# Performance work log

Measured on AMD Instinct MI355X. Metric: run time of the kernel, lower is better.

The kernel has to match this reference:

```python
import jax, jax.numpy as jnp
import numpy as np

B, S, V = 2, 336, 8      # batch, seq_len, n_vars
D, H, P = 256, 8, 96     # d_model, num_heads, pred_len
DK = D // H
OUT_CHN = 8
EPS = 1e-5


def _layernorm(x, g, b):
    mu = jnp.mean(x, axis=-1, keepdims=True)
    var = jnp.var(x, axis=-1, keepdims=True)
    return (x - mu) * jax.lax.rsqrt(var + EPS) * g + b


def _attn_ff(src, Wq, bq, Wk, bk, Wv, bv, Wo, bo, ln1_g, ln1_b):
    # src: [N, L, D]; manual MHA + residual + layernorm (dropout=0)
    N, L, _ = src.shape
    q = (src @ Wq + bq).reshape(N, L, H, DK).transpose(0, 2, 1, 3)
    k = (src @ Wk + bk).reshape(N, L, H, DK).transpose(0, 2, 1, 3)
    v = (src @ Wv + bv).reshape(N, L, H, DK).transpose(0, 2, 1, 3)
    scores = jnp.einsum('nhqd,nhkd->nhqk', q, k) / np.sqrt(DK).astype(np.float32)
    attn = jax.nn.softmax(scores, axis=-1)
    o = jnp.einsum('nhqk,nhkd->nhqd', attn, v)
    o = o.transpose(0, 2, 1, 3).reshape(N, L, D) @ Wo + bo
    return _layernorm(src + o, ln1_g, ln1_b)


def setup_inputs() -> dict:
    key = jax.random.key(0)
    ks = jax.random.split(key, 8)
    s = 1.0 / np.sqrt(D)
    return {
        'x': jax.random.normal(ks[0], (B, S, V), dtype=jnp.float32),
        'emb_w': jax.random.normal(ks[1], (1, D), dtype=jnp.float32),
        'emb_b': jnp.zeros((D,), jnp.float32),
        'Wq': jax.random.normal(ks[2], (D, D), dtype=jnp.float32) * s,
        'bq': jnp.zeros((D,), jnp.float32),
        'Wk': jax.random.normal(ks[3], (D, D), dtype=jnp.float32) * s,
        'bk': jnp.zeros((D,), jnp.float32),
        'Wv': jax.random.normal(ks[4], (D, D), dtype=jnp.float32) * s,
        'bv': jnp.zeros((D,), jnp.float32),
        'Wo': jax.random.normal(ks[5], (D, D), dtype=jnp.float32) * s,
        'bo': jnp.zeros((D,), jnp.float32),
        'ln1_g': jnp.ones((D,), jnp.float32),
        'ln1_b': jnp.zeros((D,), jnp.float32),
        'norm_g': jnp.ones((D,), jnp.float32),
        'norm_b': jnp.zeros((D,), jnp.float32),
        'proj_w': jax.random.normal(ks[6], (S * D, P), dtype=jnp.float32) / np.sqrt(S * D).astype(np.float32),
        'proj_b': jnp.zeros((P,), jnp.float32),
    }


def reference(x, emb_w, emb_b, Wq, bq, Wk, bk, Wv, bv, Wo, bo,
              ln1_g, ln1_b, norm_g, norm_b, proj_w, proj_b):
    attn_p = (Wq, bq, Wk, bk, Wv, bv, Wo, bo, ln1_g, ln1_b)
    # x: [B,S,V] -> [B,V,S] -> embed each scalar to D
    e = x.transpose(0, 2, 1)[..., None] @ emb_w + emb_b  # [B,V,S,D]
    for _ in range(10):
        # attention over time axis (shared weights)
        e = _attn_ff(e.reshape(B * V, S, D), *attn_p).reshape(B, V, S, D)
        e = _layernorm(e.transpose(0, 2, 1, 3), norm_g, norm_b)  # [B,S,V,D]
        # attention over variable axis (same weights)
        e = _attn_ff(e.reshape(B * S, V, D), *attn_p).reshape(B, S, V, D)
        e = e.transpose(0, 2, 1, 3)  # [B,V,S,D]
    out = e.reshape(B, V, S * D) @ proj_w + proj_b  # [B,V,P]
    return out.transpose(0, 2, 1)[:, :, :OUT_CHN]  # [B,P,out_chn]
```

## Files before the change

### kernel.cpp

```cpp
#include <hip/hip_runtime.h>

#define SS 336
#define VV 8
#define DD 256
#define DKK 32
#define NTOK 5376
#define NTD (NTOK * DD)
#define ATT_SCALE 0.17677669529663687f
#define LN_EPS 1e-5f

typedef _Float16 f16x8 __attribute__((ext_vector_type(8)));
typedef _Float16 f16x4v __attribute__((ext_vector_type(4)));
typedef __attribute__((ext_vector_type(4))) float f32x4;

__device__ inline _Float16 f2h(float f) { return (_Float16)f; }

__global__ __launch_bounds__(256) void k_prep_w(
    const float* __restrict__ Wq, const float* __restrict__ Wk,
    const float* __restrict__ Wv, const float* __restrict__ Wo,
    _Float16* __restrict__ WT2) {
  int z = blockIdx.y;
  const float* W = (z == 0) ? Wq : (z == 1) ? Wk : (z == 2) ? Wv : Wo;
  int o = blockIdx.x * 256 + threadIdx.x;
  int blk = o >> 9;
  int idx = o & 511;
  int lane = idx >> 3, j = idx & 7;
  int nt = blk >> 3, kb = blk & 7;
  int lcol = lane & 15, quad = lane >> 4;
  int n = nt * 16 + lcol;
  int k = kb * 32 + quad * 8 + j;
  WT2[(size_t)z * 65536 + o] = f2h(W[k * 256 + n]);
}

__global__ __launch_bounds__(256) void k_embed(
    const float* __restrict__ x, const float* __restrict__ ew,
    const float* __restrict__ eb, float* __restrict__ E,
    _Float16* __restrict__ E16) {
  int token = blockIdx.x;
  int n = token / SS, s = token - n * SS;
  int b = n >> 3, v = n & 7;
  float xv = x[(b * SS + s) * VV + v];
  int d = threadIdx.x;
  float val = fmaf(xv, ew[d], eb[d]);
  E[token * DD + d] = val;
  E16[token * DD + d] = f2h(val);
}

#define KSTR 36
#define VTSTR 344
#define PSTR 72
#define QSTR 40
__global__ __launch_bounds__(512) void k_attn_time(
    const _Float16* __restrict__ Et16, const _Float16* __restrict__ WT2,
    const float* __restrict__ bq, const float* __restrict__ bk,
    const float* __restrict__ bv, _Float16* __restrict__ O16) {
  int qg = blockIdx.x, h = blockIdx.y, n = blockIdx.z;
  int tid = threadIdx.x;
  int wave = tid >> 6, lane = tid & 63;
  int quad = lane >> 4, lcol = lane & 15;

  __shared__ __align__(16) char SMRAW[143264];
  _Float16* Ks  = (_Float16*)SMRAW;
  _Float16* Vt  = (_Float16*)(SMRAW + 24192);
  _Float16* Qs  = (_Float16*)(SMRAW + 46240);
  _Float16* Wl  = (_Float16*)(SMRAW + 60320);
  _Float16* Ach = (_Float16*)(SMRAW + 109472);
  _Float16* PsB = (_Float16*)(SMRAW + 60320);

  const size_t ebase = (size_t)(n * SS) * DD;
  const size_t base  = ebase + h * DKK;
  int qt0 = qg ? 11 : 0;
  int qtend = qg ? 21 : 11;

  const f32x4 z4 = {0.f, 0.f, 0.f, 0.f};

  {
    int h2 = h * 2;
    for (int c = tid; c < 3072; c += 512) {
      int ot = c >> 9, rest = c & 511;
      int z = (ot < 2) ? 1 : (ot < 4) ? 2 : 0;
      int nt = h2 + (ot & 1);
      *(f16x8*)&Wl[(ot << 12) + rest * 8] =
          *(const f16x8*)&WT2[(size_t)z * 65536 + nt * 4096 + rest * 8];
    }
    for (int c = tid; c < 272; c += 512) {
      if (c < 256) {
        int d = c >> 3, col = 336 + (c & 7);
        Vt[d * VTSTR + col] = (_Float16)0.f;
      } else {
        Vt[32 * VTSTR + (c - 256)] = (_Float16)0.f;
      }
    }
  }

  for (int ck = 0; ck < 6; ++ck) {
    int m0c = ck * 64;
    int nmt = (ck < 5) ? 4 : 1;
    __syncthreads();
    for (int c = tid; c < nmt * 16 * 32; c += 512) {
      int row = c >> 5, seg = c & 31;
      *(f16x8*)&Ach[row * 264 + seg * 8] =
          *(const f16x8*)&Et16[ebase + (size_t)(m0c + row) * 256 + seg * 8];
    }
    __syncthreads();
    int nU = nmt * 6;
    for (int u = wave; u < nU; u += 8) {
      int mtl = u / 6, ot = u % 6;
      int gt = ck * 4 + mtl;
      if (ot >= 4 && (gt < qt0 || gt >= qtend)) continue;
      f32x4 acc = z4;
#pragma unroll
      for (int kb = 0; kb < 8; ++kb) {
        f16x8 af = *(const f16x8*)&Ach[(mtl * 16 + lcol) * 264 + kb * 32 + quad * 8];
        f16x8 wf = *(const f16x8*)&Wl[(ot << 12) + kb * 512 + lane * 8];
        acc = __builtin_amdgcn_mfma_f32_16x16x32_f16(af, wf, acc, 0, 0, 0);
      }
      int dlo = ((ot & 1) << 4) + lcol;
      const float* bz = (ot < 2) ? bk : (ot < 4) ? bv : bq;
      float bval = bz[h * 32 + dlo];
      if (ot < 2) {
#pragma unroll
        for (int i = 0; i < 4; ++i)
          Ks[(m0c + mtl * 16 + quad * 4 + i) * KSTR + dlo] = f2h(acc[i] + bval);
      } else if (ot < 4) {
#pragma unroll
        for (int i = 0; i < 4; ++i)
          Vt[dlo * VTSTR + (m0c + mtl * 16 + quad * 4 + i)] = f2h(acc[i] + bval);
      } else {
        int ql = gt - qt0;
#pragma unroll
        for (int i = 0; i < 4; ++i)
          Qs[(ql * 16 + quad * 4 + i) * QSTR + dlo] = f2h(acc[i] + bval);
      }
    }
  }
  __syncthreads();

  _Float16* P = PsB + wave * (16 * PSTR);
  const f16x8 onesv = {(_Float16)1.f, (_Float16)1.f, (_Float16)1.f, (_Float16)1.f,
                       (_Float16)1.f, (_Float16)1.f, (_Float16)1.f, (_Float16)1.f};

  for (int qtile = qt0 + wave; qtile < qtend; qtile += 8) {
    int qb = qtile * 16;
    int ql = qtile - qt0;

    f16x8 qf = *(const f16x8*)&Qs[(ql * 16 + lcol) * QSTR + quad * 8];
    f32x4 accA = {0.f, 0.f, 0.f, 0.f};
    f32x4 accB = {0.f, 0.f, 0.f, 0.f};
    f32x4 lacc = {0.f, 0.f, 0.f, 0.f};
    float m_[4] = {-1e30f, -1e30f, -1e30f, -1e30f};

    for (int T = 0; T < 6; ++T) {
      int k0 = T * 64;
      bool full = (T < 5);
      f32x4 s[4];
      {
        const _Float16* kp = &Ks[(k0 + lcol) * KSTR + quad * 8];
        f16x4v a0 = *(const f16x4v*)kp;
        f16x4v b0 = *(const f16x4v*)(kp + 4);
        f16x8 kf = __builtin_shufflevector(a0, b0, 0, 1, 2, 3, 4, 5, 6, 7);
        s[0] = __builtin_amdgcn_mfma_f32_16x16x32_f16(qf, kf, z4, 0, 0, 0);
      }
      if (full) {
#pragma unroll
        for (int u = 1; u < 4; ++u) {
          const _Float16* kp = &Ks[(k0 + u * 16 + lcol) * KSTR + quad * 8];
          f16x4v a0 = *(const f16x4v*)kp;
          f16x4v b0 = *(const f16x4v*)(kp + 4);
          f16x8 kf = __builtin_shufflevector(a0, b0, 0, 1, 2, 3, 4, 5, 6, 7);
          s[u] = __builtin_amdgcn_mfma_f32_16x16x32_f16(qf, kf, z4, 0, 0, 0);
        }
      } else {
        s[1] = z4; s[2] = z4; s[3] = z4;
      }
      float sc[4][4], p[4][4], corr[4];
#pragma unroll
      for (int u = 0; u < 4; ++u)
#pragma unroll
        for (int i = 0; i < 4; ++i)
          sc[u][i] = (u == 0 || full) ? s[u][i] * ATT_SCALE : -1e30f;
#pragma unroll
      for (int i = 0; i < 4; ++i) {
        float t2 = fmaxf(fmaxf(sc[0][i], sc[1][i]), fmaxf(sc[2][i], sc[3][i]));
        t2 = fmaxf(t2, __shfl_xor(t2, 1));
        t2 = fmaxf(t2, __shfl_xor(t2, 2));
        t2 = fmaxf(t2, __shfl_xor(t2, 4));
        t2 = fmaxf(t2, __shfl_xor(t2, 8));
        float nm = fmaxf(m_[i], t2);
        corr[i] = __expf(m_[i] - nm);
        m_[i] = nm;
#pragma unroll
        for (int u = 0; u < 4; ++u) p[u][i] = __expf(sc[u][i] - nm);
        accA[i] *= corr[i];
        accB[i] *= corr[i];
        lacc[i] *= corr[i];
      }
#pragma unroll
      for (int i = 0; i < 4; ++i)
#pragma unroll
        for (int u = 0; u < 4; ++u)
          P[(quad * 4 + i) * PSTR + u * 16 + lcol] = f2h(p[u][i]);
      f16x8 pf0 = *(const f16x8*)&P[lcol * PSTR + quad * 8];
      lacc = __builtin_amdgcn_mfma_f32_16x16x32_f16(pf0, onesv, lacc, 0, 0, 0);
      f16x8 va0 = *(const f16x8*)&Vt[lcol * VTSTR + k0 + quad * 8];
      f16x8 vb0 = *(const f16x8*)&Vt[(16 + lcol) * VTSTR + k0 + quad * 8];
      accA = __builtin_amdgcn_mfma_f32_16x16x32_f16(pf0, va0, accA, 0, 0, 0);
      accB = __builtin_amdgcn_mfma_f32_16x16x32_f16(pf0, vb0, accB, 0, 0, 0);
      if (full) {
        f16x8 pf1 = *(const f16x8*)&P[lcol * PSTR + 32 + quad * 8];
        lacc = __builtin_amdgcn_mfma_f32_16x16x32_f16(pf1, onesv, lacc, 0, 0, 0);
        f16x8 va1 = *(const f16x8*)&Vt[lcol * VTSTR + k0 + 32 + quad * 8];
        f16x8 vb1 = *(const f16x8*)&Vt[(16 + lcol) * VTSTR + k0 + 32 + quad * 8];
        accA = __builtin_amdgcn_mfma_f32_16x16x32_f16(pf1, va1, accA, 0, 0, 0);
        accB = __builtin_amdgcn_mfma_f32_16x16x32_f16(pf1, vb1, accB, 0, 0, 0);
      }
    }

#pragma unroll
    for (int i = 0; i < 4; ++i) {
      float inv = 1.f / lacc[i];
      P[(quad * 4 + i) * PSTR + lcol] = f2h(accA[i] * inv);
      P[(quad * 4 + i) * PSTR + 16 + lcol] = f2h(accB[i] * inv);
    }
    int row = lane >> 2, seg = lane & 3;
    f16x8 ov = *(const f16x8*)&P[row * PSTR + seg * 8];
    *(f16x8*)&O16[base + (size_t)(qb + row) * DD + seg * 8] = ov;
  }
}

__global__ __launch_bounds__(512) void k_mega_var(
    const _Float16* __restrict__ AO16, const _Float16* __restrict__ WT2,
    const float* __restrict__ bq, const float* __restrict__ bk,
    const float* __restrict__ bv, const float* __restrict__ bo,
    const float* __restrict__ g1, const float* __restrict__ c1,
    const float* __restrict__ gn, const float* __restrict__ bn,
    float* __restrict__ Etime, _Float16* __restrict__ Et16) {
  int tid = threadIdx.x;
  int wave = tid >> 6, lane = tid & 63;
  int quad = lane >> 4, lcol = lane & 15;

  __shared__ int rmapS[32];
  __shared__ _Float16 Af[32 * 264];
  __shared__ float Cf[32 * 260];
  __shared__ _Float16 QKVs[32 * 776];

  if (tid < 32) {
    int r2 = blockIdx.x * 32 + tid;
    int n_idx = r2 >> 3, v = r2 & 7;
    int b = n_idx / SS, s = n_idx - b * SS;
    rmapS[tid] = (b * VV + v) * SS + s;
  }
  __syncthreads();

  {
    int row = tid >> 4, seg = tid & 15;
    const _Float16* src = AO16 + (size_t)rmapS[row] * DD + seg * 16;
    _Float16* dst = Af + row * 264 + seg * 16;
    *(f16x8*)(dst) = *(const f16x8*)(src);
    *(f16x8*)(dst + 8) = *(const f16x8*)(src + 8);
  }
  __syncthreads();

  const _Float16* WoF = WT2 + (size_t)3 * 65536;

  {
    f32x4 acc[2][2] = {};
    for (int kb = 0; kb < 8; ++kb) {
      int k0 = kb * 32;
      f16x8 af0 = *(const f16x8*)&Af[lcol * 264 + k0 + quad * 8];
      f16x8 af1 = *(const f16x8*)&Af[(16 + lcol) * 264 + k0 + quad * 8];
#pragma unroll
      for (int nt = 0; nt < 2; ++nt) {
        f16x8 bfr = *(const f16x8*)&WoF[((wave * 2 + nt) * 8 + kb) * 512 + lane * 8];
        acc[0][nt] = __builtin_amdgcn_mfma_f32_16x16x32_f16(af0, bfr, acc[0][nt], 0, 0, 0);
        acc[1][nt] = __builtin_amdgcn_mfma_f32_16x16x32_f16(af1, bfr, acc[1][nt], 0, 0, 0);
      }
    }
#pragma unroll
    for (int mt = 0; mt < 2; ++mt) {
#pragma unroll
      for (int i = 0; i < 4; ++i) {
        int row = mt * 16 + quad * 4 + i;
        size_t rb = (size_t)rmapS[row] * 256;
#pragma unroll
        for (int nt = 0; nt < 2; ++nt) {
          int col = (wave * 2 + nt) * 16 + lcol;
          Cf[row * 260 + col] = acc[mt][nt][i] + bo[col] + Etime[rb + col];
        }
      }
    }
  }
  __syncthreads();

  {
    int row = tid >> 4, c0 = (tid & 15) * 16;
    float v[16];
#pragma unroll
    for (int j = 0; j < 16; ++j) v[j] = Cf[row * 260 + c0 + j];
#pragma unroll
    for (int pass = 0; pass < 2; ++pass) {
      const float* gg = pass ? gn : g1;
      const float* bb = pass ? bn : c1;
      float s = 0.f, q = 0.f;
#pragma unroll
      for (int j = 0; j < 16; ++j) { s += v[j]; q = fmaf(v[j], v[j], q); }
      s += __shfl_xor(s, 1); q += __shfl_xor(q, 1);
      s += __shfl_xor(s, 2); q += __shfl_xor(q, 2);
      s += __shfl_xor(s, 4); q += __shfl_xor(q, 4);
      s += __shfl_xor(s, 8); q += __shfl_xor(q, 8);
      float mu = s * (1.0f / 256.0f);
      float rs = rsqrtf(q * (1.0f / 256.0f) - mu * mu + LN_EPS);
#pragma unroll
      for (int j = 0; j < 16; ++j)
        v[j] = fmaf((v[j] - mu) * rs, gg[c0 + j], bb[c0 + j]);
    }
#pragma unroll
    for (int j = 0; j < 16; ++j) Cf[row * 260 + c0 + j] = v[j];
#pragma unroll
    for (int j8 = 0; j8 < 2; ++j8) {
      f16x8 h;
#pragma unroll
      for (int jj = 0; jj < 8; ++jj) h[jj] = f2h(v[j8 * 8 + jj]);
      *(f16x8*)&Af[row * 264 + c0 + j8 * 8] = h;
    }
  }
  __syncthreads();

  {
    f32x4 acc[2][6] = {};
    for (int kb = 0; kb < 8; ++kb) {
      int k0 = kb * 32;
      f16x8 af0 = *(const f16x8*)&Af[lcol * 264 + k0 + quad * 8];
      f16x8 af1 = *(const f16x8*)&Af[(16 + lcol) * 264 + k0 + quad * 8];
#pragma unroll
      for (int j = 0; j < 6; ++j) {
        int ntg = wave * 6 + j;
        f16x8 bfr = *(const f16x8*)&WT2[(size_t)(ntg * 8 + kb) * 512 + lane * 8];
        acc[0][j] = __builtin_amdgcn_mfma_f32_16x16x32_f16(af0, bfr, acc[0][j], 0, 0, 0);
        acc[1][j] = __builtin_amdgcn_mfma_f32_16x16x32_f16(af1, bfr, acc[1][j], 0, 0, 0);
      }
    }
#pragma unroll
    for (int j = 0; j < 6; ++j) {
      int ntg = wave * 6 + j;
      int colb = ntg * 16;
      int z = colb >> 8, coln = (colb & 255) + lcol;
      const float* bz = (z == 0) ? bq : (z == 1) ? bk : bv;
      float bval = bz[coln];
#pragma unroll
      for (int mt = 0; mt < 2; ++mt) {
#pragma unroll
        for (int i = 0; i < 4; ++i)
          QKVs[(mt * 16 + quad * 4 + i) * 776 + colb + lcol] = f2h(acc[mt][j][i] + bval);
      }
    }
  }
  __syncthreads();

  {
    int half = tid & 1, qi = (tid >> 1) & 7, h = (tid >> 4) & 7, ng = tid >> 7;
    int d0 = h * 32 + half * 16;
    const _Float16* Qp = &QKVs[(ng * 8 + qi) * 776 + d0];
    float qv[16];
#pragma unroll
    for (int j8 = 0; j8 < 2; ++j8) {
      f16x8 t = *(const f16x8*)(Qp + j8 * 8);
#pragma unroll
      for (int jj = 0; jj < 8; ++jj) qv[j8 * 8 + jj] = (float)t[jj];
    }
    float sc[8];
#pragma unroll
    for (int k = 0; k < 8; ++k) {
      const _Float16* Kp = &QKVs[(ng * 8 + k) * 776 + 256 + d0];
      float s = 0.f;
#pragma unroll
      for (int j8 = 0; j8 < 2; ++j8) {
        f16x8 t = *(const f16x8*)(Kp + j8 * 8);
#pragma unroll
        for (int jj = 0; jj < 8; ++jj) s = fmaf(qv[j8 * 8 + jj], (float)t[jj], s);
      }
      sc[k] = s;
    }
#pragma unroll
    for (int k = 0; k < 8; ++k)
      sc[k] = (sc[k] + __shfl_xor(sc[k], 1)) * ATT_SCALE;
    float mx = sc[0];
#pragma unroll
    for (int k = 1; k < 8; ++k) mx = fmaxf(mx, sc[k]);
    float ps = 0.f;
#pragma unroll
    for (int k = 0; k < 8; ++k) { sc[k] = __expf(sc[k] - mx); ps += sc[k]; }
    float inv = 1.f / ps;
    float ov[16];
#pragma unroll
    for (int j = 0; j < 16; ++j) ov[j] = 0.f;
#pragma unroll
    for (int k = 0; k < 8; ++k) {
      const _Float16* Vp = &QKVs[(ng * 8 + k) * 776 + 512 + d0];
      float p = sc[k];
#pragma unroll
      for (int j8 = 0; j8 < 2; ++j8) {
        f16x8 t = *(const f16x8*)(Vp + j8 * 8);
#pragma unroll
        for (int jj = 0; jj < 8; ++jj)
          ov[j8 * 8 + jj] = fmaf(p, (float)t[jj], ov[j8 * 8 + jj]);
      }
    }
    _Float16* Op = &Af[(ng * 8 + qi) * 264 + d0];
#pragma unroll
    for (int j8 = 0; j8 < 2; ++j8) {
      f16x8 hh;
#pragma unroll
      for (int jj = 0; jj < 8; ++jj) hh[jj] = f2h(ov[j8 * 8 + jj] * inv);
      *(f16x8*)(Op + j8 * 8) = hh;
    }
  }
  __syncthreads();

  {
    f32x4 acc[2][2] = {};
    for (int kb = 0; kb < 8; ++kb) {
      int k0 = kb * 32;
      f16x8 af0 = *(const f16x8*)&Af[lcol * 264 + k0 + quad * 8];
      f16x8 af1 = *(const f16x8*)&Af[(16 + lcol) * 264 + k0 + quad * 8];
#pragma unroll
      for (int nt = 0; nt < 2; ++nt) {
        f16x8 bfr = *(const f16x8*)&WoF[((wave * 2 + nt) * 8 + kb) * 512 + lane * 8];
        acc[0][nt] = __builtin_amdgcn_mfma_f32_16x16x32_f16(af0, bfr, acc[0][nt], 0, 0, 0);
        acc[1][nt] = __builtin_amdgcn_mfma_f32_16x16x32_f16(af1, bfr, acc[1][nt], 0, 0, 0);
      }
    }
#pragma unroll
    for (int mt = 0; mt < 2; ++mt) {
#pragma unroll
      for (int i = 0; i < 4; ++i) {
        int row = mt * 16 + quad * 4 + i;
#pragma unroll
        for (int nt = 0; nt < 2; ++nt) {
          int col = (wave * 2 + nt) * 16 + lcol;
          Cf[row * 260 + col] = acc[mt][nt][i] + bo[col] + Cf[row * 260 + col];
        }
      }
    }
  }
  __syncthreads();

  {
    int row = tid >> 4, c0 = (tid & 15) * 16;
    float v[16];
#pragma unroll
    for (int j = 0; j < 16; ++j) v[j] = Cf[row * 260 + c0 + j];
    float s = 0.f, q = 0.f;
#pragma unroll
    for (int j = 0; j < 16; ++j) { s += v[j]; q = fmaf(v[j], v[j], q); }
    s += __shfl_xor(s, 1); q += __shfl_xor(q, 1);
    s += __shfl_xor(s, 2); q += __shfl_xor(q, 2);
    s += __shfl_xor(s, 4); q += __shfl_xor(q, 4);
    s += __shfl_xor(s, 8); q += __shfl_xor(q, 8);
    float mu = s * (1.0f / 256.0f);
    float rs = rsqrtf(q * (1.0f / 256.0f) - mu * mu + LN_EPS);
#pragma unroll
    for (int j = 0; j < 16; ++j)
      v[j] = fmaf((v[j] - mu) * rs, g1[c0 + j], c1[c0 + j]);
    size_t rb = (size_t)rmapS[row] * 256 + c0;
#pragma unroll
    for (int j4 = 0; j4 < 4; ++j4) {
      float4 f4 = make_float4(v[j4 * 4], v[j4 * 4 + 1], v[j4 * 4 + 2], v[j4 * 4 + 3]);
      *(float4*)&Etime[rb + j4 * 4] = f4;
    }
#pragma unroll
    for (int j8 = 0; j8 < 2; ++j8) {
      f16x8 hh;
#pragma unroll
      for (int jj = 0; jj < 8; ++jj) hh[jj] = f2h(v[j8 * 8 + jj]);
      *(f16x8*)&Et16[rb + j8 * 8] = hh;
    }
  }
}

__global__ __launch_bounds__(192) void k_proj_partial(
    const float* __restrict__ E, const float* __restrict__ PW,
    float* __restrict__ Part) {
  int kc = blockIdx.x;
  int tid = threadIdx.x;
  int p4 = tid % 24, g = tid / 24;
  __shared__ float Es[16][128];
  __shared__ float sm[8][1536];
  for (int idx = tid; idx < 512; idx += 192) {
    int row = idx >> 5, kk4 = idx & 31;
    *(float4*)&Es[row][kk4 * 4] =
        *(const float4*)&E[(size_t)row * 86016 + kc * 128 + kk4 * 4];
  }
  __syncthreads();
  float4 acc[16];
#pragma unroll
  for (int i = 0; i < 16; ++i) acc[i] = make_float4(0.f, 0.f, 0.f, 0.f);
  for (int j = 0; j < 16; ++j) {
    int k = g * 16 + j;
    float4 w = *(const float4*)&PW[(size_t)(kc * 128 + k) * 96 + p4 * 4];
#pragma unroll
    for (int row = 0; row < 16; ++row) {
      float e = Es[row][k];
      acc[row].x = fmaf(e, w.x, acc[row].x);
      acc[row].y = fmaf(e, w.y, acc[row].y);
      acc[row].z = fmaf(e, w.z, acc[row].z);
      acc[row].w = fmaf(e, w.w, acc[row].w);
    }
  }
#pragma unroll
  for (int row = 0; row < 16; ++row)
    *(float4*)&sm[g][row * 96 + p4 * 4] = acc[row];
  __syncthreads();
  for (int o = tid; o < 1536; o += 192) {
    float s = 0.f;
#pragma unroll
    for (int g2 = 0; g2 < 8; ++g2) s += sm[g2][o];
    Part[(size_t)kc * 1536 + o] = s;
  }
}

__global__ __launch_bounds__(256) void k_proj_reduce(
    const float* __restrict__ Part, const float* __restrict__ PB,
    float* __restrict__ out) {
  __shared__ float red[4][16];
  int tid = threadIdx.x;
  int j = (blockIdx.x << 4) | (tid & 15);
  int cg = tid >> 4;
  float s = 0.f;
#pragma unroll 7
  for (int i = 0; i < 42; ++i) {
    int c = cg * 42 + i;
    s += Part[(size_t)c * 1536 + j];
  }
  s += __shfl_xor(s, 16);
  s += __shfl_xor(s, 32);
  int wv = tid >> 6;
  if ((tid & 63) < 16) red[wv][tid & 15] = s;
  __syncthreads();
  if (tid < 16) {
    float t = red[0][tid] + red[1][tid] + red[2][tid] + red[3][tid];
    int jj = (blockIdx.x << 4) | tid;
    int row = jj / 96, p = jj - row * 96;
    int b = row >> 3, v = row & 7;
    out[b * 768 + p * 8 + v] = PB[p] + t;
  }
}

extern "C" void kernel_launch(void* const* d_in, const int* in_sizes, int n_in,
                              void* d_out, int out_size, void* d_ws,
                              size_t ws_size, hipStream_t stream) {
  const float* x     = (const float*)d_in[0];
  const float* emb_w = (const float*)d_in[1];
  const float* emb_b = (const float*)d_in[2];
  const float* Wq = (const float*)d_in[3];
  const float* bq = (const float*)d_in[4];
  const float* Wk = (const float*)d_in[5];
  const float* bk = (const float*)d_in[6];
  const float* Wv = (const float*)d_in[7];
  const float* bv = (const float*)d_in[8];
  const float* Wo = (const float*)d_in[9];
  const float* bo = (const float*)d_in[10];
  const float* g1 = (const float*)d_in[11];
  const float* b1 = (const float*)d_in[12];
  const float* gn = (const float*)d_in[13];
  const float* bn = (const float*)d_in[14];
  const float* PW = (const float*)d_in[15];
  const float* PB = (const float*)d_in[16];
  float* out = (float*)d_out;

  float* ws = (float*)d_ws;
  float* Etime   = ws;
  _Float16* Et16 = (_Float16*)(ws + (size_t)NTD);
  _Float16* AO16 = Et16 + (size_t)NTD;
  _Float16* WT2  = AO16 + (size_t)NTD;
  float* Part    = (float*)(WT2 + 4 * 65536);

  k_prep_w<<<dim3(256, 4), 256, 0, stream>>>(Wq, Wk, Wv, Wo, WT2);
  k_embed<<<NTOK, 256, 0, stream>>>(x, emb_w, emb_b, Etime, Et16);
  for (int it = 0; it < 10; ++it) {
    k_attn_time<<<dim3(2, 8, 16), 512, 0, stream>>>(
        Et16, WT2, bq, bk, bv, AO16);
    k_mega_var<<<168, 512, 0, stream>>>(
        AO16, WT2, bq, bk, bv, bo, g1, b1, gn, bn, Etime, Et16);
  }
  k_proj_partial<<<672, 192, 0, stream>>>(Etime, PW, Part);
  k_proj_reduce<<<96, 256, 0, stream>>>(Part, PB, out);
}
```

Baseline: 587.7 us.

## Compute next-iteration QKV in var kernel and fuse init/proj launches

The variable-attention kernel now runs the time-attention QKV projection for the next iteration at its tail. It writes Q, K and V to global memory, so the time-attention kernel only loads them, except on the first iteration, which keeps the old in-kernel projection. This stops each of the two blocks per (sequence, head) from recomputing the K/V projection, at the cost of extra global traffic for three fp16 tensors. Weight prep and embedding are merged into one launch, and the projection reduction becomes a double-precision atomic accumulation with a last-block finalize, removing two launches but adding atomics.

Result: no change. 588.2 us (+0.1%).

```diff
diff --git a/kernel.cpp b/kernel.cpp
--- a/kernel.cpp
+++ b/kernel.cpp
@@ -15,35 +15,42 @@
 
 __device__ inline _Float16 f2h(float f) { return (_Float16)f; }
 
-__global__ __launch_bounds__(256) void k_prep_w(
+__global__ __launch_bounds__(256) void k_init(
     const float* __restrict__ Wq, const float* __restrict__ Wk,
     const float* __restrict__ Wv, const float* __restrict__ Wo,
-    _Float16* __restrict__ WT2) {
-  int z = blockIdx.y;
-  const float* W = (z == 0) ? Wq : (z == 1) ? Wk : (z == 2) ? Wv : Wo;
-  int o = blockIdx.x * 256 + threadIdx.x;
-  int blk = o >> 9;
-  int idx = o & 511;
-  int lane = idx >> 3, j = idx & 7;
-  int nt = blk >> 3, kb = blk & 7;
-  int lcol = lane & 15, quad = lane >> 4;
-  int n = nt * 16 + lcol;
-  int k = kb * 32 + quad * 8 + j;
-  WT2[(size_t)z * 65536 + o] = f2h(W[k * 256 + n]);
-}
-
-__global__ __launch_bounds__(256) void k_embed(
     const float* __restrict__ x, const float* __restrict__ ew,
-    const float* __restrict__ eb, float* __restrict__ E,
-    _Float16* __restrict__ E16) {
-  int token = blockIdx.x;
-  int n = token / SS, s = token - n * SS;
-  int b = n >> 3, v = n & 7;
-  float xv = x[(b * SS + s) * VV + v];
-  int d = threadIdx.x;
-  float val = fmaf(xv, ew[d], eb[d]);
-  E[token * DD + d] = val;
-  E16[token * DD + d] = f2h(val);
+    const float* __restrict__ eb,
+    _Float16* __restrict__ WT2, float* __restrict__ E,
+    _Float16* __restrict__ E16, double* __restrict__ out64,
+    int* __restrict__ cnt) {
+  int bid = blockIdx.x;
+  int tid = threadIdx.x;
+  if (bid < 1024) {
+    int z = bid >> 8;
+    const float* W = (z == 0) ? Wq : (z == 1) ? Wk : (z == 2) ? Wv : Wo;
+    int o = (bid & 255) * 256 + tid;
+    int blk = o >> 9;
+    int idx = o & 511;
+    int lane = idx >> 3, j = idx & 7;
+    int nt = blk >> 3, kb = blk & 7;
+    int lcol = lane & 15, quad = lane >> 4;
+    int n = nt * 16 + lcol;
+    int k = kb * 32 + quad * 8 + j;
+    WT2[(size_t)z * 65536 + o] = f2h(W[k * 256 + n]);
+    if (bid == 0) {
+      for (int i = tid; i < 1536; i += 256) atomicExch(&out64[i], 0.0);
+      if (tid == 0) atomicExch(cnt, 0);
+    }
+  } else {
+    int token = bid - 1024;
+    int n = token / SS, s = token - n * SS;
+    int b = n >> 3, v = n & 7;
+    float xv = x[(b * SS + s) * VV + v];
+    int d = tid;
+    float val = fmaf(xv, ew[d], eb[d]);
+    E[token * DD + d] = val;
+    E16[token * DD + d] = f2h(val);
+  }
 }
 
 #define KSTR 36
@@ -51,9 +58,11 @@
 #define PSTR 72
 #define QSTR 40
 __global__ __launch_bounds__(512) void k_attn_time(
-    const _Float16* __restrict__ Et16, const _Float16* __restrict__ WT2,
+    const _Float16* __restrict__ Et16, const _Float16* __restrict__ Q16,
+    const _Float16* __restrict__ K16, const _Float16* __restrict__ V16,
+    const _Float16* __restrict__ WT2,
     const float* __restrict__ bq, const float* __restrict__ bk,
-    const float* __restrict__ bv, _Float16* __restrict__ O16) {
+    const float* __restrict__ bv, _Float16* __restrict__ O16, int mode) {
   int qg = blockIdx.x, h = blockIdx.y, n = blockIdx.z;
   int tid = threadIdx.x;
   int wave = tid >> 6, lane = tid & 63;
@@ -65,7 +74,7 @@
   _Float16* Qs  = (_Float16*)(SMRAW + 46240);
   _Float16* Wl  = (_Float16*)(SMRAW + 60320);
   _Float16* Ach = (_Float16*)(SMRAW + 109472);
-  _Float16* PsB = (_Float16*)(SMRAW + 60320);
+  _Float16* PsB = (_Float16*)(mode ? SMRAW + 60320 : SMRAW + 46240);
 
   const size_t ebase = (size_t)(n * SS) * DD;
   const size_t base  = ebase + h * DKK;
@@ -74,14 +83,78 @@
 
   const f32x4 z4 = {0.f, 0.f, 0.f, 0.f};
 
-  {
-    int h2 = h * 2;
-    for (int c = tid; c < 3072; c += 512) {
-      int ot = c >> 9, rest = c & 511;
-      int z = (ot < 2) ? 1 : (ot < 4) ? 2 : 0;
-      int nt = h2 + (ot & 1);
-      *(f16x8*)&Wl[(ot << 12) + rest * 8] =
-          *(const f16x8*)&WT2[(size_t)z * 65536 + nt * 4096 + rest * 8];
+  if (mode) {
+    {
+      int h2 = h * 2;
+      for (int c = tid; c < 3072; c += 512) {
+        int ot = c >> 9, rest = c & 511;
+        int z = (ot < 2) ? 1 : (ot < 4) ? 2 : 0;
+        int nt = h2 + (ot & 1);
+        *(f16x8*)&Wl[(ot << 12) + rest * 8] =
+            *(const f16x8*)&WT2[(size_t)z * 65536 + nt * 4096 + rest * 8];
+      }
+      for (int c = tid; c < 272; c += 512) {
+        if (c < 256) {
+          int d = c >> 3, col = 336 + (c & 7);
+          Vt[d * VTSTR + col] = (_Float16)0.f;
+        } else {
+          Vt[32 * VTSTR + (c - 256)] = (_Float16)0.f;
+        }
+      }
+    }
+    for (int ck = 0; ck < 6; ++ck) {
+      int m0c = ck * 64;
+      int nmt = (ck < 5) ? 4 : 1;
+      __syncthreads();
+      for (int c = tid; c < nmt * 16 * 32; c += 512) {
+        int row = c >> 5, seg = c & 31;
+        *(f16x8*)&Ach[row * 264 + seg * 8] =
+            *(const f16x8*)&Et16[ebase + (size_t)(m0c + row) * 256 + seg * 8];
+      }
+      __syncthreads();
+      int nU = nmt * 6;
+      for (int u = wave; u < nU; u += 8) {
+        int mtl = u / 6, ot = u % 6;
+        int gt = ck * 4 + mtl;
+        if (ot >= 4 && (gt < qt0 || gt >= qtend)) continue;
+        f32x4 acc = z4;
+#pragma unroll
+        for (int kb = 0; kb < 8; ++kb) {
+          f16x8 af = *(const f16x8*)&Ach[(mtl * 16 + lcol) * 264 + kb * 32 + quad * 8];
+          f16x8 wf = *(const f16x8*)&Wl[(ot << 12) + kb * 512 + lane * 8];
+          acc = __builtin_amdgcn_mfma_f32_16x16x32_f16(af, wf, acc, 0, 0, 0);
+        }
+        int dlo = ((ot & 1) << 4) + lcol;
+        const float* bz = (ot < 2) ? bk : (ot < 4) ? bv : bq;
+        float bval = bz[h * 32 + dlo];
+        if (ot < 2) {
+#pragma unroll
+          for (int i = 0; i < 4; ++i)
+            Ks[(m0c + mtl * 16 + quad * 4 + i) * KSTR + dlo] = f2h(acc[i] + bval);
+        } else if (ot < 4) {
+#pragma unroll
+          for (int i = 0; i < 4; ++i)
+            Vt[dlo * VTSTR + (m0c + mtl * 16 + quad * 4 + i)] = f2h(acc[i] + bval);
+        } else {
+          int ql = gt - qt0;
+#pragma unroll
+          for (int i = 0; i < 4; ++i)
+            Qs[(ql * 16 + quad * 4 + i) * QSTR + dlo] = f2h(acc[i] + bval);
+        }
+      }
+    }
+    __syncthreads();
+  } else {
+    for (int c = tid; c < 1344; c += 512) {
+      int row = c >> 2, part = c & 3;
+      f16x8 kv = *(const f16x8*)&K16[base + (size_t)row * DD + part * 8];
+      f16x4v klo = __builtin_shufflevector(kv, kv, 0, 1, 2, 3);
+      f16x4v khi = __builtin_shufflevector(kv, kv, 4, 5, 6, 7);
+      *(f16x4v*)&Ks[row * KSTR + part * 8] = klo;
+      *(f16x4v*)&Ks[row * KSTR + part * 8 + 4] = khi;
+      f16x8 vv = *(const f16x8*)&V16[base + (size_t)row * DD + part * 8];
+#pragma unroll
+      for (int j = 0; j < 8; ++j) Vt[(part * 8 + j) * VTSTR + row] = vv[j];
     }
     for (int c = tid; c < 272; c += 512) {
       if (c < 256) {
@@ -91,50 +164,8 @@
         Vt[32 * VTSTR + (c - 256)] = (_Float16)0.f;
       }
     }
-  }
-
-  for (int ck = 0; ck < 6; ++ck) {
-    int m0c = ck * 64;
-    int nmt = (ck < 5) ? 4 : 1;
     __syncthreads();
-    for (int c = tid; c < nmt * 16 * 32; c += 512) {
-      int row = c >> 5, seg = c & 31;
-      *(f16x8*)&Ach[row * 264 + seg * 8] =
-          *(const f16x8*)&Et16[ebase + (size_t)(m0c + row) * 256 + seg * 8];
-    }
-    __syncthreads();
-    int nU = nmt * 6;
-    for (int u = wave; u < nU; u += 8) {
-      int mtl = u / 6, ot = u % 6;
-      int gt = ck * 4 + mtl;
-      if (ot >= 4 && (gt < qt0 || gt >= qtend)) continue;
-      f32x4 acc = z4;
-#pragma unroll
-      for (int kb = 0; kb < 8; ++kb) {
-        f16x8 af = *(const f16x8*)&Ach[(mtl * 16 + lcol) * 264 + kb * 32 + quad * 8];
-        f16x8 wf = *(const f16x8*)&Wl[(ot << 12) + kb * 512 + lane * 8];
-        acc = __builtin_amdgcn_mfma_f32_16x16x32_f16(af, wf, acc, 0, 0, 0);
-      }
-      int dlo = ((ot & 1) << 4) + lcol;
-      const float* bz = (ot < 2) ? bk : (ot < 4) ? bv : bq;
-      float bval = bz[h * 32 + dlo];
-      if (ot < 2) {
-#pragma unroll
-        for (int i = 0; i < 4; ++i)
-          Ks[(m0c + mtl * 16 + quad * 4 + i) * KSTR + dlo] = f2h(acc[i] + bval);
-      } else if (ot < 4) {
-#pragma unroll
-        for (int i = 0; i < 4; ++i)
-          Vt[dlo * VTSTR + (m0c + mtl * 16 + quad * 4 + i)] = f2h(acc[i] + bval);
-      } else {
-        int ql = gt - qt0;
-#pragma unroll
-        for (int i = 0; i < 4; ++i)
-          Qs[(ql * 16 + quad * 4 + i) * QSTR + dlo] = f2h(acc[i] + bval);
-      }
-    }
-  }
-  __syncthreads();
+  }
 
   _Float16* P = PsB + wave * (16 * PSTR);
   const f16x8 onesv = {(_Float16)1.f, (_Float16)1.f, (_Float16)1.f, (_Float16)1.f,
@@ -144,7 +175,11 @@
     int qb = qtile * 16;
     int ql = qtile - qt0;
 
-    f16x8 qf = *(const f16x8*)&Qs[(ql * 16 + lcol) * QSTR + quad * 8];
+    f16x8 qf;
+    if (mode)
+      qf = *(const f16x8*)&Qs[(ql * 16 + lcol) * QSTR + quad * 8];
+    else
+      qf = *(const f16x8*)&Q16[base + (size_t)(qb + lcol) * DD + quad * 8];
     f32x4 accA = {0.f, 0.f, 0.f, 0.f};
     f32x4 accB = {0.f, 0.f, 0.f, 0.f};
     f32x4 lacc = {0.f, 0.f, 0.f, 0.f};
@@ -234,7 +269,8 @@
     const float* __restrict__ bv, const float* __restrict__ bo,
     const float* __restrict__ g1, const float* __restrict__ c1,
     const float* __restrict__ gn, const float* __restrict__ bn,
-    float* __restrict__ Etime, _Float16* __restrict__ Et16) {
+    float* __restrict__ Etime, _Float16* __restrict__ Q16,
+    _Float16* __restrict__ K16, _Float16* __restrict__ V16, int doqkv) {
   int tid = threadIdx.x;
   int wave = tid >> 6, lane = tid & 63;
   int quad = lane >> 4, lcol = lane & 15;
@@ -473,19 +509,55 @@
       f16x8 hh;
 #pragma unroll
       for (int jj = 0; jj < 8; ++jj) hh[jj] = f2h(v[j8 * 8 + jj]);
-      *(f16x8*)&Et16[rb + j8 * 8] = hh;
+      *(f16x8*)&Af[row * 264 + c0 + j8 * 8] = hh;
+    }
+  }
+  __syncthreads();
+
+  if (doqkv) {
+    f32x4 acc[2][6] = {};
+    for (int kb = 0; kb < 8; ++kb) {
+      int k0 = kb * 32;
+      f16x8 af0 = *(const f16x8*)&Af[lcol * 264 + k0 + quad * 8];
+      f16x8 af1 = *(const f16x8*)&Af[(16 + lcol) * 264 + k0 + quad * 8];
+#pragma unroll
+      for (int j = 0; j < 6; ++j) {
+        int ntg = wave * 6 + j;
+        f16x8 bfr = *(const f16x8*)&WT2[(size_t)(ntg * 8 + kb) * 512 + lane * 8];
+        acc[0][j] = __builtin_amdgcn_mfma_f32_16x16x32_f16(af0, bfr, acc[0][j], 0, 0, 0);
+        acc[1][j] = __builtin_amdgcn_mfma_f32_16x16x32_f16(af1, bfr, acc[1][j], 0, 0, 0);
+      }
+    }
+#pragma unroll
+    for (int j = 0; j < 6; ++j) {
+      int ntg = wave * 6 + j;
+      int colb = ntg * 16;
+      int z = colb >> 8, coln = (colb & 255) + lcol;
+      const float* bz = (z == 0) ? bq : (z == 1) ? bk : bv;
+      _Float16* Hd = (z == 0) ? Q16 : (z == 1) ? K16 : V16;
+      float bval = bz[coln];
+#pragma unroll
+      for (int mt = 0; mt < 2; ++mt) {
+#pragma unroll
+        for (int i = 0; i < 4; ++i) {
+          int row = mt * 16 + quad * 4 + i;
+          Hd[(size_t)rmapS[row] * 256 + coln] = f2h(acc[mt][j][i] + bval);
+        }
+      }
     }
   }
 }
 
-__global__ __launch_bounds__(192) void k_proj_partial(
+__global__ __launch_bounds__(192) void k_proj(
     const float* __restrict__ E, const float* __restrict__ PW,
-    float* __restrict__ Part) {
+    const float* __restrict__ PB, double* __restrict__ out64,
+    int* __restrict__ cnt, float* __restrict__ out) {
   int kc = blockIdx.x;
   int tid = threadIdx.x;
   int p4 = tid % 24, g = tid / 24;
   __shared__ float Es[16][128];
   __shared__ float sm[8][1536];
+  __shared__ int win;
   for (int idx = tid; idx < 512; idx += 192) {
     int row = idx >> 5, kk4 = idx & 31;
     *(float4*)&Es[row][kk4 * 4] =
@@ -515,34 +587,23 @@
     float s = 0.f;
 #pragma unroll
     for (int g2 = 0; g2 < 8; ++g2) s += sm[g2][o];
-    Part[(size_t)kc * 1536 + o] = s;
-  }
-}
-
-__global__ __launch_bounds__(256) void k_proj_reduce(
-    const float* __restrict__ Part, const float* __restrict__ PB,
-    float* __restrict__ out) {
-  __shared__ float red[4][16];
-  int tid = threadIdx.x;
-  int j = (blockIdx.x << 4) | (tid & 15);
-  int cg = tid >> 4;
-  float s = 0.f;
-#pragma unroll 7
-  for (int i = 0; i < 42; ++i) {
-    int c = cg * 42 + i;
-    s += Part[(size_t)c * 1536 + j];
-  }
-  s += __shfl_xor(s, 16);
-  s += __shfl_xor(s, 32);
-  int wv = tid >> 6;
-  if ((tid & 63) < 16) red[wv][tid & 15] = s;
-  __syncthreads();
-  if (tid < 16) {
-    float t = red[0][tid] + red[1][tid] + red[2][tid] + red[3][tid];
-    int jj = (blockIdx.x << 4) | tid;
-    int row = jj / 96, p = jj - row * 96;
-    int b = row >> 3, v = row & 7;
-    out[b * 768 + p * 8 + v] = PB[p] + t;
+    atomicAdd(&out64[o], (double)s);
+  }
+  __threadfence();
+  __syncthreads();
+  if (tid == 0) {
+    int old = atomicAdd(cnt, 1);
+    win = (old == 671) ? 1 : 0;
+  }
+  __syncthreads();
+  if (win) {
+    __threadfence();
+    for (int j = tid; j < 1536; j += 192) {
+      double t = atomicAdd(&out64[j], 0.0);
+      int row = j / 96, p = j - row * 96;
+      int b = row >> 3, v = row & 7;
+      out[b * 768 + p * 8 + v] = PB[p] + (float)t;
+    }
   }
 }
 
@@ -571,18 +632,22 @@
   float* ws = (float*)d_ws;
   float* Etime   = ws;
   _Float16* Et16 = (_Float16*)(ws + (size_t)NTD);
-  _Float16* AO16 = Et16 + (size_t)NTD;
+  _Float16* Q16  = (_Float16*)(ws + (size_t)NTD + NTD / 2);
+  _Float16* K16  = Q16 + (size_t)NTD;
+  _Float16* V16  = K16 + (size_t)NTD;
+  _Float16* AO16 = V16 + (size_t)NTD;
   _Float16* WT2  = AO16 + (size_t)NTD;
-  float* Part    = (float*)(WT2 + 4 * 65536);
-
-  k_prep_w<<<dim3(256, 4), 256, 0, stream>>>(Wq, Wk, Wv, Wo, WT2);
-  k_embed<<<NTOK, 256, 0, stream>>>(x, emb_w, emb_b, Etime, Et16);
+  double* out64  = (double*)(WT2 + 4 * 65536);
+  int* cnt       = (int*)(out64 + 1536);
+
+  k_init<<<6400, 256, 0, stream>>>(Wq, Wk, Wv, Wo, x, emb_w, emb_b,
+                                   WT2, Etime, Et16, out64, cnt);
   for (int it = 0; it < 10; ++it) {
     k_attn_time<<<dim3(2, 8, 16), 512, 0, stream>>>(
-        Et16, WT2, bq, bk, bv, AO16);
+        Et16, Q16, K16, V16, WT2, bq, bk, bv, AO16, (it == 0) ? 1 : 0);
     k_mega_var<<<168, 512, 0, stream>>>(
-        AO16, WT2, bq, bk, bv, bo, g1, b1, gn, bn, Etime, Et16);
-  }
-  k_proj_partial<<<672, 192, 0, stream>>>(Etime, PW, Part);
-  k_proj_reduce<<<96, 256, 0, stream>>>(Part, PB, out);
+        AO16, WT2, bq, bk, bv, bo, g1, b1, gn, bn, Etime,
+        Q16, K16, V16, (it < 9) ? 1 : 0);
+  }
+  k_proj<<<672, 192, 0, stream>>>(Etime, PW, PB, out64, cnt, out);
 }
```
